# Kernel optimization log

Measured on AMD Instinct MI355X. Metric: run time of the kernel, lower is better.

The kernel has to match this reference:

```python
import jax, jax.numpy as jnp
import numpy as np

BS, LX, LY, D, H, DK = 2, 2048, 2048, 1024, 16, 64


def setup_inputs() -> dict:
    key = jax.random.key(0)
    ks = jax.random.split(key, 12)
    s = 1.0 / np.sqrt(D)
    return {
        "x": jax.random.normal(ks[0], (BS, LX, D), jnp.float32),
        "y": jax.random.normal(ks[1], (BS, LY, D), jnp.float32),
        "mask": jnp.zeros((BS, 1, LX, LY), jnp.float32),
        "Wq": jax.random.normal(ks[2], (D, H * DK), jnp.float32) * s,
        "bq": jnp.zeros((H * DK,), jnp.float32),
        "Wk": jax.random.normal(ks[3], (D, H * DK), jnp.float32) * s,
        "bk": jnp.zeros((H * DK,), jnp.float32),
        "Wv": jax.random.normal(ks[4], (D, H * DK), jnp.float32) * s,
        "bv": jnp.zeros((H * DK,), jnp.float32),
        "Wo": jax.random.normal(ks[5], (H * DK, D), jnp.float32) * s,
        "bo": jnp.zeros((D,), jnp.float32),
    }


def reference(x, y, mask, Wq, bq, Wk, bk, Wv, bv, Wo, bo):
    bs, lx, _ = x.shape
    ly = y.shape[1]
    norm = DK ** 0.5
    # projections -> (bs, len, H, DK)
    q = (x @ Wq + bq).reshape(bs, lx, H, DK)
    k = (y @ Wk + bk).reshape(bs, ly, H, DK)
    v = (y @ Wv + bv).reshape(bs, ly, H, DK)
    # scores: (bs, H, lx, ly)
    scores = jnp.einsum('bxhd,byhd->bhxy', q, k) / norm + mask
    attn = jax.nn.softmax(scores, axis=-1)
    # output: (bs, lx, H, DK) -> (bs, lx, H*DK)
    out = jnp.einsum('bhxy,byhd->bxhd', attn, v).reshape(bs, lx, H * DK)
    return out @ Wo + bo
```

## Files before the change

kernel.cpp:

```cpp
#include <hip/hip_runtime.h>
#include <hip/hip_bf16.h>


typedef __bf16 bf16;
typedef __bf16 bf16x2 __attribute__((ext_vector_type(2)));
typedef __bf16 bf16x4 __attribute__((ext_vector_type(4)));
typedef __bf16 bf16x8 __attribute__((ext_vector_type(8)));
typedef float floatx4 __attribute__((ext_vector_type(4)));
typedef unsigned int uintx4 __attribute__((ext_vector_type(4)));

#define MFMA16(a, b, c) __builtin_amdgcn_mfma_f32_16x16x32_bf16(a, b, c, 0, 0, 0)

constexpr int BS = 2, LX = 2048, LY = 2048, D = 1024, H = 16, DK = 64;
constexpr int HD = H * DK;
constexpr float LOG2E = 1.4426950408889634f;

__device__ __forceinline__ void cp16(const bf16* g, bf16* l) {
  __builtin_amdgcn_global_load_lds(
      (const __attribute__((address_space(1))) unsigned int*)g,
      (__attribute__((address_space(3))) unsigned int*)l, 16, 0, 0);
}

__device__ __forceinline__ unsigned pk2(float a, float b) {
  bf16x2 p;
  p[0] = (bf16)a;
  p[1] = (bf16)b;
  return __builtin_bit_cast(unsigned, p);
}

__global__ __launch_bounds__(256) void prep(const float* __restrict__ W0, bf16* __restrict__ T0,
                                            const float* __restrict__ W1, bf16* __restrict__ T1,
                                            const float* __restrict__ W2, bf16* __restrict__ T2,
                                            const float* __restrict__ W3, bf16* __restrict__ T3,
                                            const float* __restrict__ x, bf16* __restrict__ xb,
                                            const float* __restrict__ y, bf16* __restrict__ yb,
                                            const float* __restrict__ mask, int* __restrict__ flags) {
  const int id = blockIdx.x;
  const int t = threadIdx.x;
  if (id < 1024) {
    __shared__ bf16 tile[64][72];
    const float* W;
    bf16* T;
    switch (id >> 8) {
      case 0: W = W0; T = T0; break;
      case 1: W = W1; T = T1; break;
      case 2: W = W2; T = T2; break;
      default: W = W3; T = T3; break;
    }
    const int kt = id & 15, nt = (id >> 4) & 15;
    const int r = t >> 2, c4 = (t & 3) * 16;
    const float* src = W + (size_t)(kt * 64 + r) * 1024 + nt * 64 + c4;
#pragma unroll
    for (int i = 0; i < 16; i++) tile[r][c4 + i] = (bf16)src[i];
    __syncthreads();
    bf16 vals[16];
#pragma unroll
    for (int i = 0; i < 16; i++) vals[i] = tile[c4 + i][r];
    bf16* dst = T + (size_t)(nt * 64 + r) * 1024 + kt * 64 + c4;
#pragma unroll
    for (int i = 0; i < 16; i++) dst[i] = vals[i];
  } else if (id < 5120) {
    const int id2 = id - 1024;
    const float* src = (id2 >= 2048) ? y : x;
    bf16* dst = (id2 >= 2048) ? yb : xb;
    const size_t i = ((size_t)(id2 & 2047) * 256 + t) * 8;
    float4 a = *(const float4*)(src + i);
    float4 c = *(const float4*)(src + i + 4);
    bf16 tmp[8] = {(bf16)a.x, (bf16)a.y, (bf16)a.z, (bf16)a.w,
                   (bf16)c.x, (bf16)c.y, (bf16)c.z, (bf16)c.w};
    *(bf16x8*)(dst + i) = *(const bf16x8*)tmp;
  } else {
    const int id3 = id - 5120;
    const int region = id3 >> 5, sub = id3 & 31;
    const float4* p = (const float4*)mask + (size_t)region * 65536 + sub * 2048;
    bool nz = false;
#pragma unroll
    for (int it = 0; it < 8; it++) {
      float4 v = p[it * 256 + t];
      nz |= (v.x != 0.f) | (v.y != 0.f) | (v.z != 0.f) | (v.w != 0.f);
    }
    if (nz) atomicOr(&flags[region], 1);
  }
}

__global__ __launch_bounds__(512, 2) void qkv8(const bf16* __restrict__ xb, const bf16* __restrict__ yb,
                                               const bf16* __restrict__ Wtq, const bf16* __restrict__ Wtk,
                                               const bf16* __restrict__ Wtv,
                                               const float* __restrict__ bq, const float* __restrict__ bk,
                                               const float* __restrict__ bv,
                                               bf16* __restrict__ Qb, bf16* __restrict__ Kb,
                                               bf16* __restrict__ Vt) {
  constexpr int K = 1024, N = 1024;
  __shared__ __align__(16) bf16 As[2][2][128 * 64];
  __shared__ __align__(16) bf16 Bs[2][2][128 * 64];

  const int z = blockIdx.z;
  const bf16* A = (z == 0) ? xb : yb;
  const bf16* Bt = (z == 0) ? Wtq : (z == 1) ? Wtk : Wtv;
  const float* bias = (z == 0) ? bq : (z == 1) ? bk : bv;

  const int t = threadIdx.x;
  const int w = t >> 6, lane = t & 63, quad = lane >> 4, l15 = lane & 15;
  const int wm = w >> 2, wn = w & 3;
  const int mbase = blockIdx.y * 256, nbase = blockIdx.x * 256;
  const int srow = lane >> 3, schunk = (lane & 7) ^ srow;
  const int sx = quad ^ (l15 & 7);

  floatx4 acc[2][4][2][2] = {};
  bf16x8 af[4][2];
  bf16x8 bfr[2][2][2];

#define ST_A(ktt, half, slot)                                                                 \
  {                                                                                           \
    _Pragma("unroll") for (int j = 0; j < 2; j++) {                                           \
      const int r0 = w * 16 + j * 8;                                                          \
      cp16(A + (size_t)(mbase + (half) * 128 + r0 + srow) * K + (ktt) * 64 + schunk * 8,      \
           &As[slot][half][r0 * 64]);                                                         \
    }                                                                                         \
  }
#define ST_B(ktt, half, slot)                                                                 \
  {                                                                                           \
    _Pragma("unroll") for (int j = 0; j < 2; j++) {                                           \
      const int r0 = w * 16 + j * 8;                                                          \
      cp16(Bt + (size_t)(nbase + (half) * 128 + r0 + srow) * K + (ktt) * 64 + schunk * 8,     \
           &Bs[slot][half][r0 * 64]);                                                         \
    }                                                                                         \
  }
#define LOAD_A(slot, mh)                                                                      \
  {                                                                                           \
    _Pragma("unroll") for (int i = 0; i < 4; i++) {                                           \
      const bf16* p = &As[slot][mh][(wm * 64 + i * 16 + l15) * 64];                           \
      af[i][0] = *(const bf16x8*)(p + sx * 8);                                                \
      af[i][1] = *(const bf16x8*)(p + (sx ^ 4) * 8);                                          \
    }                                                                                         \
  }
#define LOAD_B(slot, nh)                                                                      \
  {                                                                                           \
    _Pragma("unroll") for (int j = 0; j < 2; j++) {                                           \
      const bf16* p = &Bs[slot][nh][(wn * 32 + j * 16 + l15) * 64];                           \
      bfr[nh][j][0] = *(const bf16x8*)(p + sx * 8);                                           \
      bfr[nh][j][1] = *(const bf16x8*)(p + (sx ^ 4) * 8);                                     \
    }                                                                                         \
  }
#define MFMA_Q(mh, nh)                                                                        \
  {                                                                                           \
    _Pragma("unroll") for (int i = 0; i < 4; i++)                                             \
        _Pragma("unroll") for (int j = 0; j < 2; j++) {                                       \
      acc[mh][i][nh][j] = MFMA16(af[i][0], bfr[nh][j][0], acc[mh][i][nh][j]);                 \
      acc[mh][i][nh][j] = MFMA16(af[i][1], bfr[nh][j][1], acc[mh][i][nh][j]);                 \
    }                                                                                         \
  }
#define BARX()                       \
  {                                  \
    asm volatile("" ::: "memory");   \
    __builtin_amdgcn_s_barrier();    \
    asm volatile("" ::: "memory");   \
  }
#define VMW(n) asm volatile("s_waitcnt vmcnt(" #n ")" ::: "memory")
#define LG0() asm volatile("s_waitcnt lgkmcnt(0)" ::: "memory")
#define NOPST {}
#define TILE_BODY(PAR, STG0, V0, STG1, V1, STG2, STG3, V3)  \
  {                                                         \
    LOAD_A(PAR, 0);                                         \
    LOAD_B(PAR, 0);                                         \
    STG0;                                                   \
    V0;                                                     \
    BARX();                                                 \
    LG0();                                                  \
    __builtin_amdgcn_s_setprio(1);                          \
    MFMA_Q(0, 0);                                           \
    __builtin_amdgcn_s_setprio(0);                          \
    BARX();                                                 \
    LOAD_B(PAR, 1);                                         \
    STG1;                                                   \
    V1;                                                     \
    BARX();                                                 \
    LG0();                                                  \
    __builtin_amdgcn_s_setprio(1);                          \
    MFMA_Q(0, 1);                                           \
    __builtin_amdgcn_s_setprio(0);                          \
    BARX();                                                 \
    LOAD_A(PAR, 1);                                         \
    STG2;                                                   \
    BARX();                                                 \
    LG0();                                                  \
    __builtin_amdgcn_s_setprio(1);                          \
    MFMA_Q(1, 0);                                           \
    __builtin_amdgcn_s_setprio(0);                          \
    BARX();                                                 \
    STG3;                                                   \
    V3;                                                     \
    BARX();                                                 \
    LG0();                                                  \
    __builtin_amdgcn_s_setprio(1);                          \
    MFMA_Q(1, 1);                                           \
    __builtin_amdgcn_s_setprio(0);                          \
    BARX();                                                 \
  }

  ST_A(0, 0, 0);
  ST_B(0, 0, 0);
  ST_B(0, 1, 0);
  ST_A(0, 1, 0);
  ST_A(1, 0, 1);
  ST_B(1, 0, 1);
  VMW(8);
  BARX();

#pragma unroll 1
  for (int kt = 0; kt < 14; kt += 2) {
    TILE_BODY(0, ST_B(kt + 1, 1, 1), VMW(8), ST_A(kt + 1, 1, 1), VMW(8),
              ST_A(kt + 2, 0, 0), ST_B(kt + 2, 0, 0), VMW(8));
    TILE_BODY(1, ST_B(kt + 2, 1, 0), VMW(8), ST_A(kt + 2, 1, 0), VMW(8),
              ST_A(kt + 3, 0, 1), ST_B(kt + 3, 0, 1), VMW(8));
  }
  TILE_BODY(0, ST_B(15, 1, 1), VMW(8), ST_A(15, 1, 1), VMW(8), NOPST, NOPST, VMW(4));
  TILE_BODY(1, NOPST, VMW(2), NOPST, VMW(0), NOPST, NOPST, NOPST);

#undef TILE_BODY
#undef NOPST
#undef LG0
#undef VMW
#undef BARX
#undef MFMA_Q
#undef LOAD_B
#undef LOAD_A
#undef ST_B
#undef ST_A

  if (z <= 1) {
    bf16* outp = (z == 0) ? Qb : Kb;
    const float sc = (z == 0) ? 0.125f * LOG2E : 1.0f;
#pragma unroll
    for (int nh = 0; nh < 2; nh++)
#pragma unroll
      for (int j = 0; j < 2; j++) {
        const int n = nbase + nh * 128 + wn * 32 + j * 16 + l15;
        const float bv2 = bias[n];
#pragma unroll
        for (int mh = 0; mh < 2; mh++)
#pragma unroll
          for (int i = 0; i < 4; i++)
#pragma unroll
            for (int r = 0; r < 4; r++) {
              const int m = mbase + mh * 128 + wm * 64 + i * 16 + quad * 4 + r;
              outp[(size_t)m * N + n] = (bf16)((acc[mh][i][nh][j][r] + bv2) * sc);
            }
      }
  } else {
    const int b = mbase >> 11;
    const int y0 = mbase & 2047;
#pragma unroll
    for (int nh = 0; nh < 2; nh++)
#pragma unroll
      for (int j = 0; j < 2; j++) {
        const int n = nbase + nh * 128 + wn * 32 + j * 16 + l15;
        const float bv2 = bias[n];
        const int hh = n >> 6, dk = n & 63;
        bf16* dst0 = Vt + ((size_t)(b * H + hh) * DK + dk) * LY + y0;
#pragma unroll
        for (int mh = 0; mh < 2; mh++)
#pragma unroll
          for (int i = 0; i < 4; i++) {
            const int yy = mh * 128 + wm * 64 + i * 16 + quad * 4;
            bf16 tmp[4];
#pragma unroll
            for (int r = 0; r < 4; r++) tmp[r] = (bf16)(acc[mh][i][nh][j][r] + bv2);
            *(bf16x4*)(dst0 + yy) = *(const bf16x4*)tmp;
          }
      }
  }
}

__global__ __launch_bounds__(256) void out_gemm(const bf16* __restrict__ A, const bf16* __restrict__ Bt,
                                                const float* __restrict__ bias, float* __restrict__ outp) {
  constexpr int K = 1024, N = 1024;
  __shared__ __align__(16) bf16 As[128 * 64];
  __shared__ __align__(16) bf16 Bs[64 * 64];
  const int t = threadIdx.x;
  const int w = t >> 6, lane = t & 63, quad = lane >> 4, l15 = lane & 15;
  const int mbase = blockIdx.y * 128, nbase = blockIdx.x * 64;
  const int srow = lane >> 3, schunk = (lane & 7) ^ srow;
  const int sx = quad ^ (l15 & 7);

  floatx4 acc[2][4] = {};
  for (int k0 = 0; k0 < K; k0 += 64) {
    __syncthreads();
#pragma unroll
    for (int j = 0; j < 4; j++) {
      const int r0 = w * 32 + j * 8;
      cp16(A + (size_t)(mbase + r0 + srow) * K + k0 + schunk * 8, As + r0 * 64);
    }
#pragma unroll
    for (int j = 0; j < 2; j++) {
      const int r0 = w * 16 + j * 8;
      cp16(Bt + (size_t)(nbase + r0 + srow) * K + k0 + schunk * 8, Bs + r0 * 64);
    }
    __syncthreads();
    bf16x8 af[2][2], bfr[4][2];
#pragma unroll
    for (int i = 0; i < 2; i++) {
      const int ra = w * 32 + i * 16 + l15;
      af[i][0] = *(const bf16x8*)&As[ra * 64 + sx * 8];
      af[i][1] = *(const bf16x8*)&As[ra * 64 + (sx ^ 4) * 8];
    }
#pragma unroll
    for (int jn = 0; jn < 4; jn++) {
      const int rb = jn * 16 + l15;
      bfr[jn][0] = *(const bf16x8*)&Bs[rb * 64 + sx * 8];
      bfr[jn][1] = *(const bf16x8*)&Bs[rb * 64 + (sx ^ 4) * 8];
    }
#pragma unroll
    for (int i = 0; i < 2; i++)
#pragma unroll
      for (int jn = 0; jn < 4; jn++) {
        acc[i][jn] = MFMA16(af[i][0], bfr[jn][0], acc[i][jn]);
        acc[i][jn] = MFMA16(af[i][1], bfr[jn][1], acc[i][jn]);
      }
  }
#pragma unroll
  for (int jn = 0; jn < 4; jn++) {
    const int n = nbase + jn * 16 + l15;
    const float bv2 = bias[n];
#pragma unroll
    for (int i = 0; i < 2; i++)
#pragma unroll
      for (int r = 0; r < 4; r++) {
        const int m = mbase + w * 32 + i * 16 + quad * 4 + r;
        outp[(size_t)m * N + n] = acc[i][jn][r] + bv2;
      }
  }
}

__global__ __launch_bounds__(256, 4) void attn14(const bf16* __restrict__ Q, const bf16* __restrict__ Kb,
                                                 const bf16* __restrict__ Vt, const float* __restrict__ mask,
                                                 const int* __restrict__ flags, bf16* __restrict__ Hout) {
  __shared__ __align__(16) bf16 Ks[2][64 * 64];
  __shared__ __align__(16) bf16 Vs[2][64 * 64];
  const int t = threadIdx.x;
  const int w = t >> 6, lane = t & 63, quad = lane >> 4, l15 = lane & 15;
  const int xt = blockIdx.x, h = blockIdx.y, b = blockIdx.z;
  const int qbase = xt * 64 + w * 16;
  const int srow = lane >> 3, schunk = (lane & 7) ^ srow;
  const int sx = quad ^ (l15 & 7);

  bf16x8 qf[2];
  {
    const bf16* qrow = Q + (size_t)(b * LX + qbase + l15) * HD + h * DK;
    qf[0] = *(const bf16x8*)(qrow + quad * 8);
    qf[1] = *(const bf16x8*)(qrow + 32 + quad * 8);
  }
  const int mflag = flags[b * 16 + (xt >> 1)];

  bf16 onearr[8];
#pragma unroll
  for (int i = 0; i < 8; i++) onearr[i] = (bf16)((l15 == 0) ? 1.0f : 0.0f);
  const bf16x8 onesf = *(const bf16x8*)onearr;

  floatx4 o[4] = {};
  floatx4 ol = {};

  const bf16* Kbase = Kb + (size_t)b * LY * HD + h * DK;
  const bf16* Vbase = Vt + (size_t)(b * H + h) * DK * LY;
  const float* mbase2 = mask + (size_t)(b * LX + qbase + l15) * LY;

#define STAGE(yt, bufi)                                                               \
  {                                                                                   \
    _Pragma("unroll") for (int j = 0; j < 2; j++) {                                   \
      const int r0 = w * 16 + j * 8;                                                  \
      cp16(Kbase + (size_t)((yt) + r0 + srow) * HD + schunk * 8, &Ks[bufi][r0 * 64]); \
      cp16(Vbase + (size_t)(r0 + srow) * LY + (yt) + schunk * 8, &Vs[bufi][r0 * 64]); \
    }                                                                                 \
  }

#define TILE(yt, BUF)                                                                       \
  {                                                                                         \
    const bf16* KsB = Ks[BUF];                                                              \
    const bf16* VsB = Vs[BUF];                                                              \
    bf16x8 kf[4][2];                                                                        \
    _Pragma("unroll") for (int nt = 0; nt < 4; nt++) {                                      \
      const int ry = nt * 16 + l15;                                                         \
      kf[nt][0] = *(const bf16x8*)&KsB[ry * 64 + sx * 8];                                   \
      kf[nt][1] = *(const bf16x8*)&KsB[ry * 64 + (sx ^ 4) * 8];                             \
    }                                                                                       \
    floatx4 s[4];                                                                           \
    __builtin_amdgcn_s_setprio(1);                                                          \
    _Pragma("unroll") for (int nt = 0; nt < 4; nt++) {                                      \
      floatx4 sz = {0.f, 0.f, 0.f, 0.f};                                                    \
      sz = MFMA16(kf[nt][0], qf[0], sz);                                                    \
      s[nt] = MFMA16(kf[nt][1], qf[1], sz);                                                 \
    }                                                                                       \
    __builtin_amdgcn_s_setprio(0);                                                          \
    if (mflag) {                                                                            \
      _Pragma("unroll") for (int nt = 0; nt < 4; nt++) {                                    \
        const float* mp = mbase2 + (yt) + nt * 16 + quad * 4;                               \
        float4 mv = *(const float4*)mp;                                                     \
        s[nt][0] = fminf(s[nt][0] + LOG2E * mv.x, 30.f);                                    \
        s[nt][1] = fminf(s[nt][1] + LOG2E * mv.y, 30.f);                                    \
        s[nt][2] = fminf(s[nt][2] + LOG2E * mv.z, 30.f);                                    \
        s[nt][3] = fminf(s[nt][3] + LOG2E * mv.w, 30.f);                                    \
      }                                                                                     \
    }                                                                                       \
    bf16x8 pf[2];                                                                           \
    {                                                                                       \
      uintx4 wd0, wd1;                                                                      \
      _Pragma("unroll") for (int F = 0; F < 2; F++)                                         \
          _Pragma("unroll") for (int hh = 0; hh < 2; hh++) {                                \
        unsigned wa = pk2(__builtin_amdgcn_exp2f(s[2 * F][2 * hh]),                         \
                          __builtin_amdgcn_exp2f(s[2 * F][2 * hh + 1]));                    \
        unsigned wb = pk2(__builtin_amdgcn_exp2f(s[2 * F + 1][2 * hh]),                     \
                          __builtin_amdgcn_exp2f(s[2 * F + 1][2 * hh + 1]));                \
        asm("v_permlane32_swap_b32 %0, %1" : "+v"(wa), "+v"(wb));                           \
        asm("v_permlane16_swap_b32 %0, %1" : "+v"(wa), "+v"(wb));                           \
        if (F == 0) {                                                                       \
          wd0[hh] = wa;                                                                     \
          wd0[hh + 2] = wb;                                                                 \
        } else {                                                                            \
          wd1[hh] = wa;                                                                     \
          wd1[hh + 2] = wb;                                                                 \
        }                                                                                   \
      }                                                                                     \
      pf[0] = __builtin_bit_cast(bf16x8, wd0);                                              \
      pf[1] = __builtin_bit_cast(bf16x8, wd1);                                              \
    }                                                                                       \
    __builtin_amdgcn_s_setprio(1);                                                          \
    _Pragma("unroll") for (int u = 0; u < 4; u++) {                                         \
      const int rd = u * 16 + l15;                                                          \
      bf16x8 v0 = *(const bf16x8*)&VsB[rd * 64 + sx * 8];                                   \
      bf16x8 v1 = *(const bf16x8*)&VsB[rd * 64 + (sx ^ 4) * 8];                             \
      o[u] = MFMA16(pf[0], v0, o[u]);                                                       \
      o[u] = MFMA16(pf[1], v1, o[u]);                                                       \
    }                                                                                       \
    ol = MFMA16(pf[0], onesf, ol);                                                          \
    ol = MFMA16(pf[1], onesf, ol);                                                          \
    __builtin_amdgcn_s_setprio(0);                                                          \
  }

  STAGE(0, 0);
  for (int yt = 0; yt < LY; yt += 128) {
    __syncthreads();
    STAGE(yt + 64, 1);
    TILE(yt, 0);
    __syncthreads();
    if (yt + 128 < LY) STAGE(yt + 128, 0);
    TILE(yt + 64, 1);
  }

#pragma unroll
  for (int r = 0; r < 4; r++) {
    const float lsum = __shfl(ol[r], lane & 48, 64);
    const float rl = 1.0f / lsum;
    const int m = b * LX + qbase + quad * 4 + r;
#pragma unroll
    for (int u = 0; u < 4; u++)
      Hout[(size_t)m * HD + h * DK + u * 16 + l15] = (bf16)(o[u][r] * rl);
  }
#undef STAGE
#undef TILE
}

extern "C" void kernel_launch(void* const* d_in, const int* in_sizes, int n_in,
                              void* d_out, int out_size, void* d_ws, size_t ws_size,
                              hipStream_t stream) {
  const float* x = (const float*)d_in[0];
  const float* y = (const float*)d_in[1];
  const float* mask = (const float*)d_in[2];
  const float* Wq = (const float*)d_in[3];
  const float* bq = (const float*)d_in[4];
  const float* Wk = (const float*)d_in[5];
  const float* bk = (const float*)d_in[6];
  const float* Wv = (const float*)d_in[7];
  const float* bv = (const float*)d_in[8];
  const float* Wo = (const float*)d_in[9];
  const float* bo = (const float*)d_in[10];

  char* ws = (char*)d_ws;
  size_t off = 0;
  int* flags = (int*)(ws + off); off += 256;
  bf16* Qb = (bf16*)(ws + off); off += (size_t)BS * LX * HD * 2;
  bf16* Kb = (bf16*)(ws + off); off += (size_t)BS * LY * HD * 2;
  bf16* Vt = (bf16*)(ws + off); off += (size_t)BS * LY * HD * 2;
  bf16* Hb = (bf16*)(ws + off); off += (size_t)BS * LX * HD * 2;
  bf16* xbf = (bf16*)(ws + off); off += (size_t)BS * LX * D * 2;
  bf16* ybf = (bf16*)(ws + off); off += (size_t)BS * LY * D * 2;
  bf16* Wtq = (bf16*)(ws + off); off += (size_t)D * HD * 2;
  bf16* Wtk = (bf16*)(ws + off); off += (size_t)D * HD * 2;
  bf16* Wtv = (bf16*)(ws + off); off += (size_t)D * HD * 2;
  bf16* Wto = (bf16*)(ws + off); off += (size_t)HD * D * 2;

  dim3 blk(256);
  hipMemsetAsync(flags, 0, 32 * sizeof(int), stream);
  prep<<<dim3(6144), blk, 0, stream>>>(Wq, Wtq, Wk, Wtk, Wv, Wtv, Wo, Wto, x, xbf, y, ybf, mask, flags);
  qkv8<<<dim3(4, 16, 3), dim3(512), 0, stream>>>(xbf, ybf, Wtq, Wtk, Wtv, bq, bk, bv, Qb, Kb, Vt);
  attn14<<<dim3(32, 16, 2), blk, 0, stream>>>(Qb, Kb, Vt, mask, flags, Hb);
  out_gemm<<<dim3(16, 32), blk, 0, stream>>>(Hb, Wto, bo, (float*)d_out);
}
```

Before: 229.8 us.

## Double-buffer LDS fragment reads in QKV GEMM to overlap with MFMA

The QKV projection GEMM now keeps two sets of A/B register fragments. Each LDS read for the next quadrant, and for the next k-tile's first quadrant, is issued before the current MFMA block. Partial lgkmcnt waits replace full drains, so MFMA work can overlap shared-memory latency. This raises VGPR pressure under launch_bounds(512,2), and the hand-counted lgkm wait values must match the number of outstanding loads.

```diff
diff --git a/kernel.cpp b/kernel.cpp
--- a/kernel.cpp
+++ b/kernel.cpp
@@ -83,7 +83,7 @@
   }
 }
 
-__global__ __launch_bounds__(512, 2) void qkv8(const bf16* __restrict__ xb, const bf16* __restrict__ yb,
+__global__ __launch_bounds__(512, 2) void qkv9(const bf16* __restrict__ xb, const bf16* __restrict__ yb,
                                                const bf16* __restrict__ Wtq, const bf16* __restrict__ Wtk,
                                                const bf16* __restrict__ Wtv,
                                                const float* __restrict__ bq, const float* __restrict__ bk,
@@ -107,8 +107,8 @@
   const int sx = quad ^ (l15 & 7);
 
   floatx4 acc[2][4][2][2] = {};
-  bf16x8 af[4][2];
-  bf16x8 bfr[2][2][2];
+  bf16x8 afA[4][2], afB[4][2];
+  bf16x8 bfA[2][2], bfB[2][2];
 
 #define ST_A(ktt, half, slot)                                                                 \
   {                                                                                           \
@@ -126,28 +126,28 @@
            &Bs[slot][half][r0 * 64]);                                                         \
     }                                                                                         \
   }
-#define LOAD_A(slot, mh)                                                                      \
+#define LDA(slot, half, DEST)                                                                 \
   {                                                                                           \
     _Pragma("unroll") for (int i = 0; i < 4; i++) {                                           \
-      const bf16* p = &As[slot][mh][(wm * 64 + i * 16 + l15) * 64];                           \
-      af[i][0] = *(const bf16x8*)(p + sx * 8);                                                \
-      af[i][1] = *(const bf16x8*)(p + (sx ^ 4) * 8);                                          \
+      const bf16* p = &As[slot][half][(wm * 64 + i * 16 + l15) * 64];                         \
+      DEST[i][0] = *(const bf16x8*)(p + sx * 8);                                              \
+      DEST[i][1] = *(const bf16x8*)(p + (sx ^ 4) * 8);                                        \
     }                                                                                         \
   }
-#define LOAD_B(slot, nh)                                                                      \
+#define LDB(slot, half, DEST)                                                                 \
   {                                                                                           \
     _Pragma("unroll") for (int j = 0; j < 2; j++) {                                           \
-      const bf16* p = &Bs[slot][nh][(wn * 32 + j * 16 + l15) * 64];                           \
-      bfr[nh][j][0] = *(const bf16x8*)(p + sx * 8);                                           \
-      bfr[nh][j][1] = *(const bf16x8*)(p + (sx ^ 4) * 8);                                     \
+      const bf16* p = &Bs[slot][half][(wn * 32 + j * 16 + l15) * 64];                         \
+      DEST[j][0] = *(const bf16x8*)(p + sx * 8);                                              \
+      DEST[j][1] = *(const bf16x8*)(p + (sx ^ 4) * 8);                                        \
     }                                                                                         \
   }
-#define MFMA_Q(mh, nh)                                                                        \
+#define MFQ(mh, nh, AF, BF)                                                                   \
   {                                                                                           \
     _Pragma("unroll") for (int i = 0; i < 4; i++)                                             \
         _Pragma("unroll") for (int j = 0; j < 2; j++) {                                       \
-      acc[mh][i][nh][j] = MFMA16(af[i][0], bfr[nh][j][0], acc[mh][i][nh][j]);                 \
-      acc[mh][i][nh][j] = MFMA16(af[i][1], bfr[nh][j][1], acc[mh][i][nh][j]);                 \
+      acc[mh][i][nh][j] = MFMA16(AF[i][0], BF[j][0], acc[mh][i][nh][j]);                      \
+      acc[mh][i][nh][j] = MFMA16(AF[i][1], BF[j][1], acc[mh][i][nh][j]);                      \
     }                                                                                         \
   }
 #define BARX()                       \
@@ -157,43 +157,43 @@
     asm volatile("" ::: "memory");   \
   }
 #define VMW(n) asm volatile("s_waitcnt vmcnt(" #n ")" ::: "memory")
-#define LG0() asm volatile("s_waitcnt lgkmcnt(0)" ::: "memory")
+#define LGK(n) asm volatile("s_waitcnt lgkmcnt(" #n ")" ::: "memory")
 #define NOPST {}
-#define TILE_BODY(PAR, STG0, V0, STG1, V1, STG2, STG3, V3)  \
+#define RDNORM(np) { LDA(np, 0, afA); LDB(np, 0, bfA); }
+#define TILE_BODY(PAR, STG0, V0, STG1, V1, STG2, STG3, V3, RD3, LGQ3)  \
   {                                                         \
-    LOAD_A(PAR, 0);                                         \
-    LOAD_B(PAR, 0);                                         \
     STG0;                                                   \
     V0;                                                     \
     BARX();                                                 \
-    LG0();                                                  \
+    LDB(PAR, 1, bfB);                                       \
+    LGK(4);                                                 \
     __builtin_amdgcn_s_setprio(1);                          \
-    MFMA_Q(0, 0);                                           \
+    MFQ(0, 0, afA, bfA);                                    \
     __builtin_amdgcn_s_setprio(0);                          \
     BARX();                                                 \
-    LOAD_B(PAR, 1);                                         \
     STG1;                                                   \
     V1;                                                     \
     BARX();                                                 \
-    LG0();                                                  \
+    LDA(PAR, 1, afB);                                       \
+    LGK(8);                                                 \
     __builtin_amdgcn_s_setprio(1);                          \
-    MFMA_Q(0, 1);                                           \
+    MFQ(0, 1, afA, bfB);                                    \
     __builtin_amdgcn_s_setprio(0);                          \
     BARX();                                                 \
-    LOAD_A(PAR, 1);                                         \
     STG2;                                                   \
     BARX();                                                 \
-    LG0();                                                  \
+    LGK(0);                                                 \
     __builtin_amdgcn_s_setprio(1);                          \
-    MFMA_Q(1, 0);                                           \
+    MFQ(1, 0, afB, bfA);                                    \
     __builtin_amdgcn_s_setprio(0);                          \
     BARX();                                                 \
     STG3;                                                   \
     V3;                                                     \
     BARX();                                                 \
-    LG0();                                                  \
+    RD3;                                                    \
+    LGQ3;                                                   \
     __builtin_amdgcn_s_setprio(1);                          \
-    MFMA_Q(1, 1);                                           \
+    MFQ(1, 1, afB, bfB);                                    \
     __builtin_amdgcn_s_setprio(0);                          \
     BARX();                                                 \
   }
@@ -206,25 +206,28 @@
   ST_B(1, 0, 1);
   VMW(8);
   BARX();
+  RDNORM(0);
 
 #pragma unroll 1
   for (int kt = 0; kt < 14; kt += 2) {
     TILE_BODY(0, ST_B(kt + 1, 1, 1), VMW(8), ST_A(kt + 1, 1, 1), VMW(8),
-              ST_A(kt + 2, 0, 0), ST_B(kt + 2, 0, 0), VMW(8));
+              ST_A(kt + 2, 0, 0), ST_B(kt + 2, 0, 0), VMW(8), RDNORM(1), LGK(12));
     TILE_BODY(1, ST_B(kt + 2, 1, 0), VMW(8), ST_A(kt + 2, 1, 0), VMW(8),
-              ST_A(kt + 3, 0, 1), ST_B(kt + 3, 0, 1), VMW(8));
-  }
-  TILE_BODY(0, ST_B(15, 1, 1), VMW(8), ST_A(15, 1, 1), VMW(8), NOPST, NOPST, VMW(4));
-  TILE_BODY(1, NOPST, VMW(2), NOPST, VMW(0), NOPST, NOPST, NOPST);
+              ST_A(kt + 3, 0, 1), ST_B(kt + 3, 0, 1), VMW(8), RDNORM(0), LGK(12));
+  }
+  TILE_BODY(0, ST_B(15, 1, 1), VMW(8), ST_A(15, 1, 1), VMW(8), NOPST, NOPST, VMW(4),
+            RDNORM(1), LGK(12));
+  TILE_BODY(1, NOPST, VMW(2), NOPST, VMW(0), NOPST, NOPST, NOPST, NOPST, LGK(0));
 
 #undef TILE_BODY
+#undef RDNORM
 #undef NOPST
-#undef LG0
+#undef LGK
 #undef VMW
 #undef BARX
-#undef MFMA_Q
-#undef LOAD_B
-#undef LOAD_A
+#undef MFQ
+#undef LDB
+#undef LDA
 #undef ST_B
 #undef ST_A
 
@@ -491,7 +494,7 @@
   dim3 blk(256);
   hipMemsetAsync(flags, 0, 32 * sizeof(int), stream);
   prep<<<dim3(6144), blk, 0, stream>>>(Wq, Wtq, Wk, Wtk, Wv, Wtv, Wo, Wto, x, xbf, y, ybf, mask, flags);
-  qkv8<<<dim3(4, 16, 3), dim3(512), 0, stream>>>(xbf, ybf, Wtq, Wtk, Wtv, bq, bk, bv, Qb, Kb, Vt);
+  qkv9<<<dim3(4, 16, 3), dim3(512), 0, stream>>>(xbf, ybf, Wtq, Wtk, Wtv, bq, bk, bv, Qb, Kb, Vt);
   attn14<<<dim3(32, 16, 2), blk, 0, stream>>>(Qb, Kb, Vt, mask, flags, Hb);
   out_gemm<<<dim3(16, 32), blk, 0, stream>>>(Hb, Wto, bo, (float*)d_out);
 }
```

Measured after the change: 250.1 us. 8.8% more time.
